# Performance work log

Measured on AMD Instinct MI355X. Metric: run time of the kernel, lower is better.

## Reference

```python
import jax, jax.numpy as jnp
import numpy as np

EPS = 1e-5
GROUPS = 32


def conv2d(x, w, b):
    # x: [N,C,H,W], w: [O,I,3,3] (or 1x1), stride 1, padding 'same' for 3x3
    kh = w.shape[2]
    pad = (kh - 1) // 2
    y = jax.lax.conv_general_dilated(x, w, (1, 1), ((pad, pad), (pad, pad)),
                                     dimension_numbers=('NCHW', 'OIHW', 'NCHW'))
    return y + b[None, :, None, None]


def group_norm(x, g, b):
    N, C, H, W = x.shape
    xr = x.reshape(N, GROUPS, C // GROUPS, H, W)
    mu = xr.mean(axis=(2, 3, 4), keepdims=True)
    var = xr.var(axis=(2, 3, 4), keepdims=True)
    xr = (xr - mu) / jnp.sqrt(var + EPS)
    return xr.reshape(N, C, H, W) * g[None, :, None, None] + b[None, :, None, None]


def batch_norm(x, g, b):
    # training-mode BatchNorm2d: batch statistics over (N,H,W)
    mu = x.mean(axis=(0, 2, 3), keepdims=True)
    var = x.var(axis=(0, 2, 3), keepdims=True)
    return (x - mu) / jnp.sqrt(var + EPS) * g[None, :, None, None] + b[None, :, None, None]


def binary_activation(x):
    # STE: forward sign(x), backward through piecewise poly out3
    out_fwd = jnp.sign(x)
    m1 = (x < -1).astype(x.dtype)
    m2 = (x < 0).astype(x.dtype)
    m3 = (x < 1).astype(x.dtype)
    out1 = -1.0 * m1 + (x * x + 2.0 * x) * (1.0 - m1)
    out2 = out1 * m2 + (-x * x + 2.0 * x) * (1.0 - m2)
    out3 = out2 * m3 + 1.0 * (1.0 - m3)
    return jax.lax.stop_gradient(out_fwd - out3) + out3


def hard_binary_conv(x, w, b):
    # per-output-channel scaling * sign(w), STE through clipped weights
    scale = jax.lax.stop_gradient(jnp.mean(jnp.abs(w), axis=(1, 2, 3), keepdims=True))
    bw_ng = scale * jnp.sign(w)
    clipped = jnp.clip(w, -1.0, 1.0)
    bw = jax.lax.stop_gradient(bw_ng - clipped) + clipped
    return conv2d(x, bw, b)


def learnable_bias(x, emb, w, b):
    bias = jax.nn.silu(emb) @ w.T + b  # [B, C]
    return x + bias[:, :, None, None]


def _forward(c, x, emb,
             rb_gn1_g, rb_gn1_b, rb_conv1_w, rb_conv1_b, rb_emb_w, rb_emb_b,
             rb_gn2_g, rb_gn2_b, rb_conv2_w, rb_conv2_b,
             m1_w, m1_b, bconv_w, bconv_b, bn_g, bn_b,
             m2_w, m2_b, prelu_a, m3_w, m3_b):
    # ResBlock (skip = Identity since out_channels == channels)
    h = conv2d(jax.nn.silu(group_norm(c, rb_gn1_g, rb_gn1_b)), rb_conv1_w, rb_conv1_b)
    eo = jax.nn.silu(emb) @ rb_emb_w.T + rb_emb_b          # [B, 2*C]
    scale, shift = jnp.split(eo[:, :, None, None], 2, axis=1)
    h = group_norm(h, rb_gn2_g, rb_gn2_b) * (1.0 + scale) + shift
    h = conv2d(jax.nn.silu(h), rb_conv2_w, rb_conv2_b)
    c2 = c + h
    # concat + bias + STE binarize + binary conv + BN + channel-pool residual + PReLU
    xc = jnp.concatenate([x, c2], axis=1)                   # [B, 2C, H, W]
    out = learnable_bias(xc, emb, m1_w, m1_b)
    out = binary_activation(out)
    out = hard_binary_conv(out, bconv_w, bconv_b)
    out = batch_norm(out, bn_g, bn_b)
    N, C2, H, W = xc.shape
    out = out + xc.reshape(N, C2 // 2, 2, H, W).mean(axis=2)  # channel mean pooling
    out = learnable_bias(out, emb, m2_w, m2_b)
    out = jnp.where(out >= 0, out, prelu_a[None, :, None, None] * out)  # PReLU
    out = learnable_bias(out, emb, m3_w, m3_b)
    return out


def setup_inputs() -> dict:
    key = jax.random.key(0)
    ks = jax.random.split(key, 24)
    B, C, EMB, H, W = 8, 128, 512, 64, 64
    IN2 = 2 * C
    n = lambda k, s, sc=0.05: jax.random.normal(k, s, dtype=jnp.float32) * sc
    return {
        'c': jax.random.normal(ks[0], (B, C, H, W), dtype=jnp.float32),
        'x': jax.random.normal(ks[1], (B, C, H, W), dtype=jnp.float32),
        'emb': jax.random.normal(ks[2], (B, EMB), dtype=jnp.float32),
        'rb_gn1_g': jnp.ones((C,), jnp.float32), 'rb_gn1_b': jnp.zeros((C,), jnp.float32),
        'rb_conv1_w': n(ks[3], (C, C, 3, 3)), 'rb_conv1_b': n(ks[4], (C,)),
        'rb_emb_w': n(ks[5], (2 * C, EMB)), 'rb_emb_b': n(ks[6], (2 * C,)),
        'rb_gn2_g': jnp.ones((C,), jnp.float32), 'rb_gn2_b': jnp.zeros((C,), jnp.float32),
        'rb_conv2_w': n(ks[7], (C, C, 3, 3)), 'rb_conv2_b': n(ks[8], (C,)),
        'm1_w': n(ks[9], (IN2, EMB)), 'm1_b': n(ks[10], (IN2,)),
        'bconv_w': jax.random.uniform(ks[11], (C, IN2, 3, 3), dtype=jnp.float32) * 0.001,
        'bconv_b': n(ks[12], (C,)),
        'bn_g': jnp.ones((C,), jnp.float32), 'bn_b': jnp.zeros((C,), jnp.float32),
        'm2_w': n(ks[13], (C, EMB)), 'm2_b': n(ks[14], (C,)),
        'prelu_a': jnp.full((C,), 0.25, jnp.float32),
        'm3_w': n(ks[15], (C, EMB)), 'm3_b': n(ks[16], (C,)),
    }


def reference(c, x, emb,
              rb_gn1_g, rb_gn1_b, rb_conv1_w, rb_conv1_b, rb_emb_w, rb_emb_b,
              rb_gn2_g, rb_gn2_b, rb_conv2_w, rb_conv2_b,
              m1_w, m1_b, bconv_w, bconv_b, bn_g, bn_b,
              m2_w, m2_b, prelu_a, m3_w, m3_b):
    return _forward(c, x, emb,
                    rb_gn1_g, rb_gn1_b, rb_conv1_w, rb_conv1_b, rb_emb_w, rb_emb_b,
                    rb_gn2_g, rb_gn2_b, rb_conv2_w, rb_conv2_b,
                    m1_w, m1_b, bconv_w, bconv_b, bn_g, bn_b,
                    m2_w, m2_b, prelu_a, m3_w, m3_b)
```

## Files before the change

kernel.cpp:

```cpp
#include <hip/hip_runtime.h>
#include <stdint.h>


#define B_   8
#define C_   128
#define C2_  256
#define HW_  4096
#define EMB_ 512
#define EPS_ 1e-5f

typedef int   v16i __attribute__((ext_vector_type(16)));
typedef float v16f __attribute__((ext_vector_type(16)));
typedef short v8s  __attribute__((ext_vector_type(8)));
typedef int   v4i  __attribute__((ext_vector_type(4)));

#define COLB 272
#define LDSZ (3 * 66 * COLB)

__device__ __forceinline__ float silu(float v) { return v / (1.f + expf(-v)); }
__device__ __forceinline__ unsigned short f2bf(float f) {
    unsigned int x = __float_as_uint(f);
    return (unsigned short)((x + 0x7FFFu + ((x >> 16) & 1u)) >> 16);
}
__device__ __forceinline__ int8_t sgn8(float v) {
    return (v > 0.f) ? (int8_t)1 : ((v < 0.f) ? (int8_t)(-1) : (int8_t)0);
}

__global__ __launch_bounds__(256) void k_prep(
    const float* __restrict__ w, int8_t* __restrict__ sgn,
    float* __restrict__ alpha, float* __restrict__ bnS, float* __restrict__ bnQ,
    float* __restrict__ gnS, float* __restrict__ gnQ,
    const float* __restrict__ w1, const float* __restrict__ w2,
    unsigned short* __restrict__ Wc1, unsigned short* __restrict__ Wc2,
    const float* __restrict__ emb,
    const float* __restrict__ ew, const float* __restrict__ ebb,
    const float* __restrict__ m1w, const float* __restrict__ m1b,
    const float* __restrict__ m2w, const float* __restrict__ m2b,
    const float* __restrict__ m3w, const float* __restrict__ m3b,
    float* __restrict__ eo, float* __restrict__ b1,
    float* __restrict__ b2, float* __restrict__ b3) {
    __shared__ float red[256];
    const int blk = blockIdx.x, tid = threadIdx.x;
    if (blk < 128) {
        const int o = blk;
        if (o == 0 && tid < 128) { bnS[tid] = 0.f; bnQ[tid] = 0.f; }
        if (o == 1) { gnS[tid] = 0.f; }
        if (o == 2) { gnQ[tid] = 0.f; }
        const float* wr = w + (size_t)o * (C2_ * 9);
        float s = 0.f;
        for (int i = tid; i < C2_ * 9; i += 256) s += fabsf(wr[i]);
        red[tid] = s;
        __syncthreads();
        for (int st = 128; st > 0; st >>= 1) {
            if (tid < st) red[tid] += red[tid + st];
            __syncthreads();
        }
        if (tid == 0) alpha[o] = red[0] / (float)(C2_ * 9);
        for (int kk = 0; kk < 9; ++kk) {
            float v = wr[tid * 9 + kk];
            sgn[((size_t)(kk * 16 + (tid >> 4)) * C_ + o) * 16 + (tid & 15)] = sgn8(v);
        }
    } else if (blk < 704) {
        int i = (blk - 128) * 256 + tid;
        int co = i / (C_ * 9);
        int rem = i - co * (C_ * 9);
        int ci = rem / 9, kk = rem - ci * 9;
        size_t d = ((size_t)(kk * 16 + (ci >> 3)) * C_ + co) * 8 + (ci & 7);
        Wc1[d] = f2bf(w1[i]);
        Wc2[d] = f2bf(w2[i]);
    } else {
        const int o = (blk - 704) * 4 + (tid >> 6);
        const int l = tid & 63;
        const float* wv;
        float bias;
        float* dst;
        int dstride;
        if (o < 256)      { wv = ew  + (size_t)o * EMB_;              bias = ebb[o];    dst = eo + o;  dstride = 256; }
        else if (o < 512) { int r = o - 256; wv = m1w + (size_t)r * EMB_; bias = m1b[r]; dst = b1 + r; dstride = 256; }
        else if (o < 640) { int r = o - 512; wv = m2w + (size_t)r * EMB_; bias = m2b[r]; dst = b2 + r; dstride = 128; }
        else              { int r = o - 640; wv = m3w + (size_t)r * EMB_; bias = m3b[r]; dst = b3 + r; dstride = 128; }
        const float4 wa = *(const float4*)(wv + 8 * l);
        const float4 wb = *(const float4*)(wv + 8 * l + 4);
#pragma unroll
        for (int b = 0; b < B_; ++b) {
            const float* s = emb + b * EMB_ + 8 * l;
            float4 sa = *(const float4*)(s);
            float4 sb = *(const float4*)(s + 4);
            float p = wa.x * silu(sa.x) + wa.y * silu(sa.y) + wa.z * silu(sa.z) + wa.w * silu(sa.w) +
                      wb.x * silu(sb.x) + wb.y * silu(sb.y) + wb.z * silu(sb.z) + wb.w * silu(sb.w);
#pragma unroll
            for (int off = 32; off > 0; off >>= 1) p += __shfl_down(p, off, 64);
            if (l == 0) dst[b * dstride] = bias + p;
        }
    }
}

__global__ __launch_bounds__(1024) void k_gn1t(const float* __restrict__ in,
                                               const float* __restrict__ g,
                                               const float* __restrict__ b,
                                               unsigned short* __restrict__ act) {
    __shared__ float ssum[1024], ssq[1024];
    __shared__ float s_mu, s_rstd;
    const int tid = threadIdx.x;
    const int n = blockIdx.x >> 5, grp = blockIdx.x & 31;
    const size_t base = ((size_t)(n * C_ + grp * 4)) << 12;
    float sum = 0.f, sq = 0.f;
    const float4* in4 = (const float4*)(in + base);
    for (int i = tid; i < 4096; i += 1024) {
        float4 v = in4[i];
        sum += v.x + v.y + v.z + v.w;
        sq += v.x * v.x + v.y * v.y + v.z * v.z + v.w * v.w;
    }
    ssum[tid] = sum; ssq[tid] = sq;
    __syncthreads();
    for (int st = 512; st > 0; st >>= 1) {
        if (tid < st) { ssum[tid] += ssum[tid + st]; ssq[tid] += ssq[tid + st]; }
        __syncthreads();
    }
    if (tid == 0) {
        float mu = ssum[0] * (1.f / 16384.f);
        float var = ssq[0] * (1.f / 16384.f) - mu * mu;
        s_mu = mu; s_rstd = rsqrtf(var + EPS_);
    }
    __syncthreads();
    const float mu = s_mu, rstd = s_rstd;
    float gg[4], bb[4];
#pragma unroll
    for (int j = 0; j < 4; ++j) { gg[j] = g[grp * 4 + j]; bb[j] = b[grp * 4 + j]; }
    for (int hw = tid; hw < HW_; hw += 1024) {
        union { unsigned short u[4]; uint2 v; } pk;
#pragma unroll
        for (int j = 0; j < 4; ++j) {
            float v = in[base + ((size_t)j << 12) + hw];
            pk.u[j] = f2bf(silu((v - mu) * rstd * gg[j] + bb[j]));
        }
        *(uint2*)(act + ((size_t)(n * HW_ + hw)) * C_ + grp * 4) = pk.v;
    }
}

__global__ __launch_bounds__(1024) void k_gn2a(const float* __restrict__ in,
                                               const float* __restrict__ g,
                                               const float* __restrict__ b,
                                               const float* __restrict__ eo,
                                               const float* __restrict__ gnS,
                                               const float* __restrict__ gnQ,
                                               unsigned short* __restrict__ act) {
    const int tid = threadIdx.x;
    const int n = blockIdx.x >> 5, grp = blockIdx.x & 31;
    const size_t base = ((size_t)(n * C_ + grp * 4)) << 12;
    const float mu = gnS[n * 32 + grp] * (1.f / 16384.f);
    const float var = gnQ[n * 32 + grp] * (1.f / 16384.f) - mu * mu;
    const float rstd = rsqrtf(var + EPS_);
    float sc[4], sh[4], gg[4], bb[4];
#pragma unroll
    for (int j = 0; j < 4; ++j) {
        int ch = grp * 4 + j;
        gg[j] = g[ch]; bb[j] = b[ch];
        sc[j] = 1.f + eo[n * 256 + ch];
        sh[j] = eo[n * 256 + 128 + ch];
    }
    for (int hw = tid; hw < HW_; hw += 1024) {
        union { unsigned short u[4]; uint2 v; } pk;
#pragma unroll
        for (int j = 0; j < 4; ++j) {
            float v = in[base + ((size_t)j << 12) + hw];
            float y = ((v - mu) * rstd * gg[j] + bb[j]) * sc[j] + sh[j];
            pk.u[j] = f2bf(silu(y));
        }
        *(uint2*)(act + ((size_t)(n * HW_ + hw)) * C_ + grp * 4) = pk.v;
    }
}

__device__ __forceinline__ void stage_rows(char* lds, const char* rs0,
                                           const char* rs1, const char* rs2) {
    const int tid = threadIdx.x;
    const char* rs[3] = {rs0, rs1, rs2};
    if (tid < 96) {
        int r = tid / 32, q = tid & 31;
        int c = (q >> 4) ? 65 : 0, o = q & 15;
        *(float4*)(lds + (r * 66 + c) * COLB + o * 16) = make_float4(0.f, 0.f, 0.f, 0.f);
    }
#pragma unroll
    for (int u = 0; u < 12; ++u) {
        int idx = u * 256 + tid;
        int r = idx >> 10, rem = idx & 1023;
        int x = rem >> 4, o = rem & 15;
        char* dst = lds + (r * 66 + x + 1) * COLB + o * 16;
        if (rs[r]) *(float4*)dst = *(const float4*)(rs[r] + x * 256 + o * 16);
        else       *(float4*)dst = make_float4(0.f, 0.f, 0.f, 0.f);
    }
}

__global__ __launch_bounds__(256) void k_conv1(const unsigned short* __restrict__ act,
                                               const unsigned short* __restrict__ Wc,
                                               const float* __restrict__ bias,
                                               float* __restrict__ out,
                                               float* __restrict__ gnS,
                                               float* __restrict__ gnQ) {
    __shared__ __align__(16) char lds[LDSZ];
    const int y = blockIdx.x;
    const int n = blockIdx.y;
    const char* base = (const char*)(act + ((size_t)n * 64) * 64 * C_);
    stage_rows(lds,
               (y > 0)  ? base + (size_t)(y - 1) * 16384 : nullptr,
               base + (size_t)y * 16384,
               (y < 63) ? base + (size_t)(y + 1) * 16384 : nullptr);
    __syncthreads();

    const int w = threadIdx.x >> 6;
    const int l = threadIdx.x & 63;
    const int lm = l & 31;
    const int lh = l >> 5;

    v16f acc0, acc1;
#pragma unroll
    for (int i = 0; i < 16; ++i) { acc0[i] = 0.f; acc1[i] = 0.f; }

#pragma unroll
    for (int kk = 0; kk < 9; ++kk) {
        const int r = kk / 3, dx = kk % 3 - 1;
        const char* col0 = lds + (r * 66 + lm + 1 + dx) * COLB + 16 * lh;
        const char* col1 = col0 + 32 * COLB;
        const unsigned short* wbase = Wc + (size_t)(kk * 16 + lh) * C_ * 8 + (32 * w + lm) * 8;
#pragma unroll
        for (int cb = 0; cb < 8; ++cb) {
            v8s a = *(const v8s*)(wbase + (size_t)(2 * cb) * C_ * 8);
            v8s b0 = *(const v8s*)(col0 + 32 * cb);
            v8s b1 = *(const v8s*)(col1 + 32 * cb);
            acc0 = __builtin_amdgcn_mfma_f32_32x32x16_bf16(a, b0, acc0, 0, 0, 0);
            acc1 = __builtin_amdgcn_mfma_f32_32x32x16_bf16(a, b1, acc1, 0, 0, 0);
        }
    }
    float pr[16], qr[16];
#pragma unroll
    for (int r = 0; r < 16; ++r) {
        const int row = (r & 3) + 8 * (r >> 2) + 4 * lh;
        const int co = 32 * w + row;
        const float bv = bias[co];
        const size_t o = (((size_t)n * C_ + co) << 12) + (y << 6);
        float v0 = acc0[r] + bv, v1 = acc1[r] + bv;
        out[o + lm] = v0;
        out[o + 32 + lm] = v1;
        pr[r] = v0 + v1;
        qr[r] = v0 * v0 + v1 * v1;
    }
    __syncthreads();
    float* ldsS = (float*)lds;
    float* ldsQ = (float*)lds + 128;
#pragma unroll
    for (int r = 0; r < 16; ++r) {
        float p = pr[r], q = qr[r];
#pragma unroll
        for (int m = 16; m > 0; m >>= 1) {
            p += __shfl_xor(p, m, 64);
            q += __shfl_xor(q, m, 64);
        }
        if (lm == 0) {
            const int row = (r & 3) + 8 * (r >> 2) + 4 * lh;
            const int co = 32 * w + row;
            ldsS[co] = p;
            ldsQ[co] = q;
        }
    }
    __syncthreads();
    if (threadIdx.x < 32) {
        const int g = threadIdx.x;
        float p = ldsS[4 * g] + ldsS[4 * g + 1] + ldsS[4 * g + 2] + ldsS[4 * g + 3];
        float q = ldsQ[4 * g] + ldsQ[4 * g + 1] + ldsQ[4 * g + 2] + ldsQ[4 * g + 3];
        atomicAdd(&gnS[n * 32 + g], p);
        atomicAdd(&gnQ[n * 32 + g], q);
    }
}

__global__ __launch_bounds__(256) void k_conv2(const unsigned short* __restrict__ act,
                                               const unsigned short* __restrict__ Wc,
                                               const float* __restrict__ bias,
                                               const float* __restrict__ res,
                                               const float* __restrict__ xin,
                                               const float* __restrict__ b1v,
                                               float* __restrict__ out,
                                               int8_t* __restrict__ S) {
    __shared__ __align__(16) char lds[LDSZ];
    const int y = blockIdx.x;
    const int n = blockIdx.y;
    const char* base = (const char*)(act + ((size_t)n * 64) * 64 * C_);
    stage_rows(lds,
               (y > 0)  ? base + (size_t)(y - 1) * 16384 : nullptr,
               base + (size_t)y * 16384,
               (y < 63) ? base + (size_t)(y + 1) * 16384 : nullptr);
    __syncthreads();

    const int w = threadIdx.x >> 6;
    const int l = threadIdx.x & 63;
    const int lm = l & 31;
    const int lh = l >> 5;

    v16f acc0, acc1;
#pragma unroll
    for (int i = 0; i < 16; ++i) { acc0[i] = 0.f; acc1[i] = 0.f; }

#pragma unroll
    for (int kk = 0; kk < 9; ++kk) {
        const int r = kk / 3, dx = kk % 3 - 1;
        const char* col0 = lds + (r * 66 + lm + 1 + dx) * COLB + 16 * lh;
        const char* col1 = col0 + 32 * COLB;
        const unsigned short* wbase = Wc + (size_t)(kk * 16 + lh) * C_ * 8 + (32 * w + lm) * 8;
#pragma unroll
        for (int cb = 0; cb < 8; ++cb) {
            v8s a = *(const v8s*)(wbase + (size_t)(2 * cb) * C_ * 8);
            v8s b0 = *(const v8s*)(col0 + 32 * cb);
            v8s b1 = *(const v8s*)(col1 + 32 * cb);
            acc0 = __builtin_amdgcn_mfma_f32_32x32x16_bf16(a, b0, acc0, 0, 0, 0);
            acc1 = __builtin_amdgcn_mfma_f32_32x32x16_bf16(a, b1, acc1, 0, 0, 0);
        }
    }
    float c2v0[16], c2v1[16];
#pragma unroll
    for (int r = 0; r < 16; ++r) {
        const int row = (r & 3) + 8 * (r >> 2) + 4 * lh;
        const int co = 32 * w + row;
        const float bv = bias[co];
        const size_t o = (((size_t)n * C_ + co) << 12) + (y << 6);
        float v0 = acc0[r] + bv + res[o + lm];
        float v1 = acc1[r] + bv + res[o + 32 + lm];
        out[o + lm] = v0;
        out[o + 32 + lm] = v1;
        c2v0[r] = v0;
        c2v1[r] = v1;
    }

    __syncthreads();
#pragma unroll
    for (int q = 0; q < 4; ++q) {
        const int co0 = 32 * w + 8 * q + 4 * lh;
        const float b0 = b1v[n * 256 + 128 + co0];
        const float b1b = b1v[n * 256 + 128 + co0 + 1];
        const float b2b = b1v[n * 256 + 128 + co0 + 2];
        const float b3b = b1v[n * 256 + 128 + co0 + 3];
        union { int8_t b[4]; int u; } p0, p1;
        p0.b[0] = sgn8(c2v0[4 * q] + b0);  p1.b[0] = sgn8(c2v1[4 * q] + b0);
        p0.b[1] = sgn8(c2v0[4 * q + 1] + b1b); p1.b[1] = sgn8(c2v1[4 * q + 1] + b1b);
        p0.b[2] = sgn8(c2v0[4 * q + 2] + b2b); p1.b[2] = sgn8(c2v1[4 * q + 2] + b2b);
        p0.b[3] = sgn8(c2v0[4 * q + 3] + b3b); p1.b[3] = sgn8(c2v1[4 * q + 3] + b3b);
        *(int*)(lds + lm * COLB + 128 + co0) = p0.u;
        *(int*)(lds + (32 + lm) * COLB + 128 + co0) = p1.u;
    }
#pragma unroll
    for (int u = 0; u < 8; ++u) {
        int idx = u * 256 + threadIdx.x;
        int ch = idx >> 4, seg = idx & 15;
        float4 v = *(const float4*)(xin + (((size_t)(n * C_ + ch)) << 12) + (y << 6) + 4 * seg);
        const float bv = b1v[n * 256 + ch];
        lds[(4 * seg) * COLB + ch]     = sgn8(v.x + bv);
        lds[(4 * seg + 1) * COLB + ch] = sgn8(v.y + bv);
        lds[(4 * seg + 2) * COLB + ch] = sgn8(v.z + bv);
        lds[(4 * seg + 3) * COLB + ch] = sgn8(v.w + bv);
    }
    __syncthreads();
    int8_t* Srow = S + ((size_t)(n * HW_) + (y << 6)) * C2_;
#pragma unroll
    for (int u = 0; u < 4; ++u) {
        int idx = u * 256 + threadIdx.x;
        int px = idx >> 4, c16 = idx & 15;
        *(int4*)(Srow + (size_t)px * C2_ + 16 * c16) = *(const int4*)(lds + px * COLB + 16 * c16);
    }
}

__global__ __launch_bounds__(256) void k_bconv(const int8_t* __restrict__ S,
                                               const int8_t* __restrict__ Wk,
                                               const float* __restrict__ alpha,
                                               const float* __restrict__ bias,
                                               float* __restrict__ out,
                                               float* __restrict__ bnS,
                                               float* __restrict__ bnQ) {
    __shared__ __align__(16) char lds[LDSZ];
    const int y = blockIdx.x;
    const int n = blockIdx.y;
    const char* base = (const char*)(S + ((size_t)n * 64) * 64 * C2_);
    stage_rows(lds,
               (y > 0)  ? base + (size_t)(y - 1) * 16384 : nullptr,
               base + (size_t)y * 16384,
               (y < 63) ? base + (size_t)(y + 1) * 16384 : nullptr);
    __syncthreads();

    const int w = threadIdx.x >> 6;
    const int l = threadIdx.x & 63;
    const int lm = l & 31;
    const int lh = l >> 5;

    v16i acc0, acc1;
#pragma unroll
    for (int i = 0; i < 16; ++i) { acc0[i] = 0; acc1[i] = 0; }

#pragma unroll
    for (int kk = 0; kk < 9; ++kk) {
        const int r = kk / 3, dx = kk % 3 - 1;
        const char* col0 = lds + (r * 66 + lm + 1 + dx) * COLB + 16 * lh;
        const char* col1 = col0 + 32 * COLB;
        const int8_t* wbase = Wk + (size_t)(kk * 16 + lh) * C_ * 16 + (32 * w + lm) * 16;
#pragma unroll
        for (int s = 0; s < 8; ++s) {
            v4i a = *(const v4i*)(wbase + (size_t)(2 * s) * C_ * 16);
            v4i b0 = *(const v4i*)(col0 + 32 * s);
            v4i b1 = *(const v4i*)(col1 + 32 * s);
            acc0 = __builtin_amdgcn_mfma_i32_32x32x32_i8(a, b0, acc0, 0, 0, 0);
            acc1 = __builtin_amdgcn_mfma_i32_32x32x32_i8(a, b1, acc1, 0, 0, 0);
        }
    }

    float pr[16], qr[16];
#pragma unroll
    for (int r = 0; r < 16; ++r) {
        const int row = (r & 3) + 8 * (r >> 2) + 4 * lh;
        const int co = 32 * w + row;
        const float av = alpha[co], bv = bias[co];
        const size_t o = (((size_t)n * C_ + co) << 12) + (y << 6);
        float v0 = av * (float)acc0[r] + bv;
        float v1 = av * (float)acc1[r] + bv;
        out[o + lm]      = v0;
        out[o + 32 + lm] = v1;
        pr[r] = v0 + v1;
        qr[r] = v0 * v0 + v1 * v1;
    }
    __syncthreads();
    float* ldsS = (float*)lds;
    float* ldsQ = (float*)lds + 128;
#pragma unroll
    for (int r = 0; r < 16; ++r) {
        float p = pr[r], q = qr[r];
#pragma unroll
        for (int m = 16; m > 0; m >>= 1) {
            p += __shfl_xor(p, m, 64);
            q += __shfl_xor(q, m, 64);
        }
        if (lm == 0) {
            const int row = (r & 3) + 8 * (r >> 2) + 4 * lh;
            const int co = 32 * w + row;
            ldsS[co] = p;
            ldsQ[co] = q;
        }
    }
    __syncthreads();
    if (threadIdx.x < 128) {
        atomicAdd(&bnS[threadIdx.x], ldsS[threadIdx.x]);
        atomicAdd(&bnQ[threadIdx.x], ldsQ[threadIdx.x]);
    }
}

__global__ __launch_bounds__(256) void k_final(const float* __restrict__ y3,
                                               const float* __restrict__ x,
                                               const float* __restrict__ c2,
                                               const float* __restrict__ bnS,
                                               const float* __restrict__ bnQ,
                                               const float* __restrict__ bng,
                                               const float* __restrict__ bnb,
                                               const float* __restrict__ b2v,
                                               const float* __restrict__ pa,
                                               const float* __restrict__ b3v,
                                               float* __restrict__ out) {
    const int idx4 = blockIdx.x * 256 + threadIdx.x;
    const int hw = (idx4 & 1023) * 4;
    const int cb = idx4 >> 10;
    const int co = cb & 127;
    const int n = cb >> 7;
    const float mu = bnS[co] * (1.f / 32768.f);
    const float var = bnQ[co] * (1.f / 32768.f) - mu * mu;
    const float rstd = rsqrtf(var + EPS_);
    const float gm = rstd * bng[co];
    const float bt = bnb[co] - mu * gm;
    const size_t obase = (((size_t)(n * C_ + co)) << 12) + hw;
    float4 v = *(const float4*)(y3 + obase);
    v.x = v.x * gm + bt; v.y = v.y * gm + bt; v.z = v.z * gm + bt; v.w = v.w * gm + bt;

    const int ch0 = 2 * co;
    float4 pA, pB;
    if (co < 64) {
        pA = *(const float4*)(x + (((size_t)(n * C_ + ch0)) << 12) + hw);
        pB = *(const float4*)(x + (((size_t)(n * C_ + ch0 + 1)) << 12) + hw);
    } else {
        int d = ch0 - 128;
        pA = *(const float4*)(c2 + (((size_t)(n * C_ + d)) << 12) + hw);
        pB = *(const float4*)(c2 + (((size_t)(n * C_ + d + 1)) << 12) + hw);
    }
    const float bias2 = b2v[n * 128 + co];
    const float aP = pa[co];
    const float bias3 = b3v[n * 128 + co];
    float4 r;
    float t;
    t = v.x + 0.5f * (pA.x + pB.x) + bias2; t = (t >= 0.f) ? t : aP * t; r.x = t + bias3;
    t = v.y + 0.5f * (pA.y + pB.y) + bias2; t = (t >= 0.f) ? t : aP * t; r.y = t + bias3;
    t = v.z + 0.5f * (pA.z + pB.z) + bias2; t = (t >= 0.f) ? t : aP * t; r.z = t + bias3;
    t = v.w + 0.5f * (pA.w + pB.w) + bias2; t = (t >= 0.f) ? t : aP * t; r.w = t + bias3;
    *(float4*)(out + obase) = r;
}

extern "C" void kernel_launch(void* const* d_in, const int* in_sizes, int n_in,
                              void* d_out, int out_size, void* d_ws, size_t ws_size,
                              hipStream_t stream) {
    const float* c       = (const float*)d_in[0];
    const float* x       = (const float*)d_in[1];
    const float* emb     = (const float*)d_in[2];
    const float* gn1_g   = (const float*)d_in[3];
    const float* gn1_b   = (const float*)d_in[4];
    const float* conv1_w = (const float*)d_in[5];
    const float* conv1_b = (const float*)d_in[6];
    const float* emb_w   = (const float*)d_in[7];
    const float* emb_b   = (const float*)d_in[8];
    const float* gn2_g   = (const float*)d_in[9];
    const float* gn2_b   = (const float*)d_in[10];
    const float* conv2_w = (const float*)d_in[11];
    const float* conv2_b = (const float*)d_in[12];
    const float* m1_w    = (const float*)d_in[13];
    const float* m1_b    = (const float*)d_in[14];
    const float* bconv_w = (const float*)d_in[15];
    const float* bconv_b = (const float*)d_in[16];
    const float* bn_g    = (const float*)d_in[17];
    const float* bn_b    = (const float*)d_in[18];
    const float* m2_w    = (const float*)d_in[19];
    const float* m2_b    = (const float*)d_in[20];
    const float* prelu_a = (const float*)d_in[21];
    const float* m3_w    = (const float*)d_in[22];
    const float* m3_b    = (const float*)d_in[23];
    float* out = (float*)d_out;

    float* ws = (float*)d_ws;
    const size_t NCHW = (size_t)B_ * C_ * HW_;
    float*  a_buf = ws;
    float*  y_buf = ws + NCHW;
    unsigned short* actA = (unsigned short*)(ws + 2 * NCHW);
    int8_t* S     = (int8_t*)(ws + 2 * NCHW);
    int8_t* sgn   = (int8_t*)(ws + 2 * NCHW + NCHW / 2);
    unsigned short* Wc1 = (unsigned short*)(ws + 2 * NCHW + NCHW / 2 + 73728);
    unsigned short* Wc2 = Wc1 + C_ * C_ * 9;
    float*  alpha = ws + 2 * NCHW + NCHW / 2 + 73728 + 2 * 73728;
    float*  eo    = alpha + 128;
    float*  b1v   = eo + B_ * 256;
    float*  b2v   = b1v + B_ * 256;
    float*  b3v   = b2v + B_ * 128;
    float*  bnS   = b3v + B_ * 128;
    float*  bnQ   = bnS + 128;
    float*  gnS   = bnQ + 128;
    float*  gnQ   = gnS + 256;

    k_prep<<<896, 256, 0, stream>>>(bconv_w, sgn, alpha, bnS, bnQ, gnS, gnQ,
                                    conv1_w, conv2_w, Wc1, Wc2,
                                    emb, emb_w, emb_b, m1_w, m1_b, m2_w, m2_b,
                                    m3_w, m3_b, eo, b1v, b2v, b3v);
    k_gn1t<<<B_ * 32, 1024, 0, stream>>>(c, gn1_g, gn1_b, actA);
    k_conv1<<<dim3(64, B_), 256, 0, stream>>>(actA, Wc1, conv1_b, y_buf, gnS, gnQ);
    k_gn2a<<<B_ * 32, 1024, 0, stream>>>(y_buf, gn2_g, gn2_b, eo, gnS, gnQ, actA);
    k_conv2<<<dim3(64, B_), 256, 0, stream>>>(actA, Wc2, conv2_b, c, x, b1v, a_buf, S);
    k_bconv<<<dim3(64, B_), 256, 0, stream>>>(S, sgn, alpha, bconv_b, y_buf, bnS, bnQ);
    k_final<<<NCHW / 1024, 256, 0, stream>>>(y_buf, x, a_buf, bnS, bnQ, bn_g, bn_b,
                                             b2v, prelu_a, b3v, out);
}
```

Before: 257.7 us.

## Fuse GroupNorm kernels into prep and conv2 staging, store pooled conv2 output

GroupNorm1+SiLU moves into extra blocks of the prep kernel. GroupNorm2 with its emb modulation and SiLU is folded into conv2's LDS staging, which reads fp32 conv1 output directly, so two launches and an intermediate bf16 activation round-trip go away. Conv2 now writes a channel-pair-pooled half-size buffer instead of the full output, and SiLU uses a fast exp and reciprocal. Risks: the gn1 blocks in prep now run alongside the weight repacking, conv2 staging does more strided fp32 loads, and the fast-math SiLU is slightly less accurate.

```diff
diff --git a/kernel.cpp b/kernel.cpp
--- a/kernel.cpp
+++ b/kernel.cpp
@@ -17,7 +17,9 @@
 #define COLB 272
 #define LDSZ (3 * 66 * COLB)
 
-__device__ __forceinline__ float silu(float v) { return v / (1.f + expf(-v)); }
+__device__ __forceinline__ float silu(float v) {
+    return v * __builtin_amdgcn_rcpf(1.f + __expf(-v));
+}
 __device__ __forceinline__ unsigned short f2bf(float f) {
     unsigned int x = __float_as_uint(f);
     return (unsigned short)((x + 0x7FFFu + ((x >> 16) & 1u)) >> 16);
@@ -38,7 +40,9 @@
     const float* __restrict__ m2w, const float* __restrict__ m2b,
     const float* __restrict__ m3w, const float* __restrict__ m3b,
     float* __restrict__ eo, float* __restrict__ b1,
-    float* __restrict__ b2, float* __restrict__ b3) {
+    float* __restrict__ b2, float* __restrict__ b3,
+    const float* __restrict__ gin, const float* __restrict__ g1w,
+    const float* __restrict__ g1b, unsigned short* __restrict__ act1) {
     __shared__ float red[256];
     const int blk = blockIdx.x, tid = threadIdx.x;
     if (blk < 128) {
@@ -68,7 +72,7 @@
         size_t d = ((size_t)(kk * 16 + (ci >> 3)) * C_ + co) * 8 + (ci & 7);
         Wc1[d] = f2bf(w1[i]);
         Wc2[d] = f2bf(w2[i]);
-    } else {
+    } else if (blk < 896) {
         const int o = (blk - 704) * 4 + (tid >> 6);
         const int l = tid & 63;
         const float* wv;
@@ -92,82 +96,40 @@
             for (int off = 32; off > 0; off >>= 1) p += __shfl_down(p, off, 64);
             if (l == 0) dst[b * dstride] = bias + p;
         }
-    }
-}
-
-__global__ __launch_bounds__(1024) void k_gn1t(const float* __restrict__ in,
-                                               const float* __restrict__ g,
-                                               const float* __restrict__ b,
-                                               unsigned short* __restrict__ act) {
-    __shared__ float ssum[1024], ssq[1024];
-    __shared__ float s_mu, s_rstd;
-    const int tid = threadIdx.x;
-    const int n = blockIdx.x >> 5, grp = blockIdx.x & 31;
-    const size_t base = ((size_t)(n * C_ + grp * 4)) << 12;
-    float sum = 0.f, sq = 0.f;
-    const float4* in4 = (const float4*)(in + base);
-    for (int i = tid; i < 4096; i += 1024) {
-        float4 v = in4[i];
-        sum += v.x + v.y + v.z + v.w;
-        sq += v.x * v.x + v.y * v.y + v.z * v.z + v.w * v.w;
-    }
-    ssum[tid] = sum; ssq[tid] = sq;
-    __syncthreads();
-    for (int st = 512; st > 0; st >>= 1) {
-        if (tid < st) { ssum[tid] += ssum[tid + st]; ssq[tid] += ssq[tid + st]; }
+    } else {
+        const int bb = blk - 896;
+        const int n = bb >> 5, grp = bb & 31;
+        const size_t base = ((size_t)(n * C_ + grp * 4)) << 12;
+        float sum = 0.f, sq = 0.f;
+        const float4* in4 = (const float4*)(gin + base);
+        for (int i = tid; i < 4096; i += 256) {
+            float4 v = in4[i];
+            sum += v.x + v.y + v.z + v.w;
+            sq += v.x * v.x + v.y * v.y + v.z * v.z + v.w * v.w;
+        }
+#pragma unroll
+        for (int off = 32; off > 0; off >>= 1) {
+            sum += __shfl_xor(sum, off, 64);
+            sq  += __shfl_xor(sq, off, 64);
+        }
+        if ((tid & 63) == 0) { red[tid >> 6] = sum; red[8 + (tid >> 6)] = sq; }
         __syncthreads();
-    }
-    if (tid == 0) {
-        float mu = ssum[0] * (1.f / 16384.f);
-        float var = ssq[0] * (1.f / 16384.f) - mu * mu;
-        s_mu = mu; s_rstd = rsqrtf(var + EPS_);
-    }
-    __syncthreads();
-    const float mu = s_mu, rstd = s_rstd;
-    float gg[4], bb[4];
-#pragma unroll
-    for (int j = 0; j < 4; ++j) { gg[j] = g[grp * 4 + j]; bb[j] = b[grp * 4 + j]; }
-    for (int hw = tid; hw < HW_; hw += 1024) {
-        union { unsigned short u[4]; uint2 v; } pk;
-#pragma unroll
-        for (int j = 0; j < 4; ++j) {
-            float v = in[base + ((size_t)j << 12) + hw];
-            pk.u[j] = f2bf(silu((v - mu) * rstd * gg[j] + bb[j]));
-        }
-        *(uint2*)(act + ((size_t)(n * HW_ + hw)) * C_ + grp * 4) = pk.v;
-    }
-}
-
-__global__ __launch_bounds__(1024) void k_gn2a(const float* __restrict__ in,
-                                               const float* __restrict__ g,
-                                               const float* __restrict__ b,
-                                               const float* __restrict__ eo,
-                                               const float* __restrict__ gnS,
-                                               const float* __restrict__ gnQ,
-                                               unsigned short* __restrict__ act) {
-    const int tid = threadIdx.x;
-    const int n = blockIdx.x >> 5, grp = blockIdx.x & 31;
-    const size_t base = ((size_t)(n * C_ + grp * 4)) << 12;
-    const float mu = gnS[n * 32 + grp] * (1.f / 16384.f);
-    const float var = gnQ[n * 32 + grp] * (1.f / 16384.f) - mu * mu;
-    const float rstd = rsqrtf(var + EPS_);
-    float sc[4], sh[4], gg[4], bb[4];
-#pragma unroll
-    for (int j = 0; j < 4; ++j) {
-        int ch = grp * 4 + j;
-        gg[j] = g[ch]; bb[j] = b[ch];
-        sc[j] = 1.f + eo[n * 256 + ch];
-        sh[j] = eo[n * 256 + 128 + ch];
-    }
-    for (int hw = tid; hw < HW_; hw += 1024) {
-        union { unsigned short u[4]; uint2 v; } pk;
-#pragma unroll
-        for (int j = 0; j < 4; ++j) {
-            float v = in[base + ((size_t)j << 12) + hw];
-            float y = ((v - mu) * rstd * gg[j] + bb[j]) * sc[j] + sh[j];
-            pk.u[j] = f2bf(silu(y));
-        }
-        *(uint2*)(act + ((size_t)(n * HW_ + hw)) * C_ + grp * 4) = pk.v;
+        sum = red[0] + red[1] + red[2] + red[3];
+        sq  = red[8] + red[9] + red[10] + red[11];
+        const float mu = sum * (1.f / 16384.f);
+        const float rstd = rsqrtf(sq * (1.f / 16384.f) - mu * mu + EPS_);
+        float gg[4], bb4[4];
+#pragma unroll
+        for (int j = 0; j < 4; ++j) { gg[j] = g1w[grp * 4 + j]; bb4[j] = g1b[grp * 4 + j]; }
+        for (int hw = tid; hw < HW_; hw += 256) {
+            union { unsigned short u[4]; uint2 v; } pk;
+#pragma unroll
+            for (int j = 0; j < 4; ++j) {
+                float v = gin[base + ((size_t)j << 12) + hw];
+                pk.u[j] = f2bf(silu((v - mu) * rstd * gg[j] + bb4[j]));
+            }
+            *(uint2*)(act1 + ((size_t)(n * HW_ + hw)) * C_ + grp * 4) = pk.v;
+        }
     }
 }
 
@@ -272,26 +234,66 @@
     }
 }
 
-__global__ __launch_bounds__(256) void k_conv2(const unsigned short* __restrict__ act,
+__global__ __launch_bounds__(256) void k_conv2(const float* __restrict__ yin,
                                                const unsigned short* __restrict__ Wc,
                                                const float* __restrict__ bias,
                                                const float* __restrict__ res,
                                                const float* __restrict__ xin,
                                                const float* __restrict__ b1v,
-                                               float* __restrict__ out,
+                                               const float* __restrict__ eo,
+                                               const float* __restrict__ g2,
+                                               const float* __restrict__ bt2,
+                                               const float* __restrict__ gnS,
+                                               const float* __restrict__ gnQ,
+                                               float* __restrict__ poolC2,
                                                int8_t* __restrict__ S) {
     __shared__ __align__(16) char lds[LDSZ];
+    __shared__ float ldsA[128], ldsB[128];
     const int y = blockIdx.x;
     const int n = blockIdx.y;
-    const char* base = (const char*)(act + ((size_t)n * 64) * 64 * C_);
-    stage_rows(lds,
-               (y > 0)  ? base + (size_t)(y - 1) * 16384 : nullptr,
-               base + (size_t)y * 16384,
-               (y < 63) ? base + (size_t)(y + 1) * 16384 : nullptr);
-    __syncthreads();
-
-    const int w = threadIdx.x >> 6;
-    const int l = threadIdx.x & 63;
+    const int tid = threadIdx.x;
+
+    if (tid < 128) {
+        const int ch = tid, grp = tid >> 2;
+        const float mu = gnS[n * 32 + grp] * (1.f / 16384.f);
+        const float var = gnQ[n * 32 + grp] * (1.f / 16384.f) - mu * mu;
+        const float rstd = rsqrtf(var + EPS_);
+        const float gg = g2[ch] * rstd;
+        const float sc = 1.f + eo[n * 256 + ch];
+        ldsA[ch] = gg * sc;
+        ldsB[ch] = (bt2[ch] - mu * gg) * sc + eo[n * 256 + 128 + ch];
+    }
+    if (tid < 96) {
+        int r = tid / 32, q = tid & 31;
+        int cpad = (q >> 4) ? 65 : 0, o = q & 15;
+        *(float4*)(lds + (r * 66 + cpad) * COLB + o * 16) = make_float4(0.f, 0.f, 0.f, 0.f);
+    }
+    __syncthreads();
+
+    const float* yb = yin + ((size_t)n * C_) * HW_ + (y << 6);
+#pragma unroll 4
+    for (int u = 0; u < 24; ++u) {
+        int unit = u * 256 + tid;
+        int r = unit >> 11, rem = unit & 2047;
+        int ch = rem >> 4, seg = rem & 15;
+        int yy = y - 1 + r;
+        char* dst = lds + (r * 66 + 1 + seg) * COLB + ch * 2;
+        if (yy >= 0 && yy < 64) {
+            const float A = ldsA[ch], Bv = ldsB[ch];
+            const float* src = yb + (size_t)ch * HW_ + (r - 1) * 64 + seg;
+#pragma unroll
+            for (int j = 0; j < 4; ++j)
+                *(unsigned short*)(dst + (16 * j) * COLB) = f2bf(silu(src[16 * j] * A + Bv));
+        } else {
+#pragma unroll
+            for (int j = 0; j < 4; ++j)
+                *(unsigned short*)(dst + (16 * j) * COLB) = 0;
+        }
+    }
+    __syncthreads();
+
+    const int w = tid >> 6;
+    const int l = tid & 63;
     const int lm = l & 31;
     const int lh = l >> 5;
 
@@ -321,12 +323,17 @@
         const int co = 32 * w + row;
         const float bv = bias[co];
         const size_t o = (((size_t)n * C_ + co) << 12) + (y << 6);
-        float v0 = acc0[r] + bv + res[o + lm];
-        float v1 = acc1[r] + bv + res[o + 32 + lm];
-        out[o + lm] = v0;
-        out[o + 32 + lm] = v1;
-        c2v0[r] = v0;
-        c2v1[r] = v1;
+        c2v0[r] = acc0[r] + bv + res[o + lm];
+        c2v1[r] = acc1[r] + bv + res[o + 32 + lm];
+    }
+#pragma unroll
+    for (int q = 0; q < 4; ++q) {
+        const int pc = 16 * w + 4 * q + 2 * lh;
+        const size_t po = (((size_t)n * 64 + pc) << 12) + (y << 6);
+        poolC2[po + lm]             = 0.5f * (c2v0[4 * q] + c2v0[4 * q + 1]);
+        poolC2[po + 32 + lm]        = 0.5f * (c2v1[4 * q] + c2v1[4 * q + 1]);
+        poolC2[po + 4096 + lm]      = 0.5f * (c2v0[4 * q + 2] + c2v0[4 * q + 3]);
+        poolC2[po + 4096 + 32 + lm] = 0.5f * (c2v1[4 * q + 2] + c2v1[4 * q + 3]);
     }
 
     __syncthreads();
@@ -347,7 +354,7 @@
     }
 #pragma unroll
     for (int u = 0; u < 8; ++u) {
-        int idx = u * 256 + threadIdx.x;
+        int idx = u * 256 + tid;
         int ch = idx >> 4, seg = idx & 15;
         float4 v = *(const float4*)(xin + (((size_t)(n * C_ + ch)) << 12) + (y << 6) + 4 * seg);
         const float bv = b1v[n * 256 + ch];
@@ -360,7 +367,7 @@
     int8_t* Srow = S + ((size_t)(n * HW_) + (y << 6)) * C2_;
 #pragma unroll
     for (int u = 0; u < 4; ++u) {
-        int idx = u * 256 + threadIdx.x;
+        int idx = u * 256 + tid;
         int px = idx >> 4, c16 = idx & 15;
         *(int4*)(Srow + (size_t)px * C2_ + 16 * c16) = *(const int4*)(lds + px * COLB + 16 * c16);
     }
@@ -449,7 +456,7 @@
 
 __global__ __launch_bounds__(256) void k_final(const float* __restrict__ y3,
                                                const float* __restrict__ x,
-                                               const float* __restrict__ c2,
+                                               const float* __restrict__ poolC2,
                                                const float* __restrict__ bnS,
                                                const float* __restrict__ bnQ,
                                                const float* __restrict__ bng,
@@ -472,25 +479,25 @@
     float4 v = *(const float4*)(y3 + obase);
     v.x = v.x * gm + bt; v.y = v.y * gm + bt; v.z = v.z * gm + bt; v.w = v.w * gm + bt;
 
-    const int ch0 = 2 * co;
-    float4 pA, pB;
+    float4 pv;
     if (co < 64) {
-        pA = *(const float4*)(x + (((size_t)(n * C_ + ch0)) << 12) + hw);
-        pB = *(const float4*)(x + (((size_t)(n * C_ + ch0 + 1)) << 12) + hw);
+        const int ch0 = 2 * co;
+        float4 pA = *(const float4*)(x + (((size_t)(n * C_ + ch0)) << 12) + hw);
+        float4 pB = *(const float4*)(x + (((size_t)(n * C_ + ch0 + 1)) << 12) + hw);
+        pv.x = 0.5f * (pA.x + pB.x); pv.y = 0.5f * (pA.y + pB.y);
+        pv.z = 0.5f * (pA.z + pB.z); pv.w = 0.5f * (pA.w + pB.w);
     } else {
-        int d = ch0 - 128;
-        pA = *(const float4*)(c2 + (((size_t)(n * C_ + d)) << 12) + hw);
-        pB = *(const float4*)(c2 + (((size_t)(n * C_ + d + 1)) << 12) + hw);
+        pv = *(const float4*)(poolC2 + (((size_t)(n * 64 + co - 64)) << 12) + hw);
     }
     const float bias2 = b2v[n * 128 + co];
     const float aP = pa[co];
     const float bias3 = b3v[n * 128 + co];
     float4 r;
     float t;
-    t = v.x + 0.5f * (pA.x + pB.x) + bias2; t = (t >= 0.f) ? t : aP * t; r.x = t + bias3;
-    t = v.y + 0.5f * (pA.y + pB.y) + bias2; t = (t >= 0.f) ? t : aP * t; r.y = t + bias3;
-    t = v.z + 0.5f * (pA.z + pB.z) + bias2; t = (t >= 0.f) ? t : aP * t; r.z = t + bias3;
-    t = v.w + 0.5f * (pA.w + pB.w) + bias2; t = (t >= 0.f) ? t : aP * t; r.w = t + bias3;
+    t = v.x + pv.x + bias2; t = (t >= 0.f) ? t : aP * t; r.x = t + bias3;
+    t = v.y + pv.y + bias2; t = (t >= 0.f) ? t : aP * t; r.y = t + bias3;
+    t = v.z + pv.z + bias2; t = (t >= 0.f) ? t : aP * t; r.z = t + bias3;
+    t = v.w + pv.w + bias2; t = (t >= 0.f) ? t : aP * t; r.w = t + bias3;
     *(float4*)(out + obase) = r;
 }
 
@@ -525,7 +532,7 @@
 
     float* ws = (float*)d_ws;
     const size_t NCHW = (size_t)B_ * C_ * HW_;
-    float*  a_buf = ws;
+    float*  poolC2 = ws;
     float*  y_buf = ws + NCHW;
     unsigned short* actA = (unsigned short*)(ws + 2 * NCHW);
     int8_t* S     = (int8_t*)(ws + 2 * NCHW);
@@ -542,15 +549,15 @@
     float*  gnS   = bnQ + 128;
     float*  gnQ   = gnS + 256;
 
-    k_prep<<<896, 256, 0, stream>>>(bconv_w, sgn, alpha, bnS, bnQ, gnS, gnQ,
-                                    conv1_w, conv2_w, Wc1, Wc2,
-                                    emb, emb_w, emb_b, m1_w, m1_b, m2_w, m2_b,
-                                    m3_w, m3_b, eo, b1v, b2v, b3v);
-    k_gn1t<<<B_ * 32, 1024, 0, stream>>>(c, gn1_g, gn1_b, actA);
+    k_prep<<<1152, 256, 0, stream>>>(bconv_w, sgn, alpha, bnS, bnQ, gnS, gnQ,
+                                     conv1_w, conv2_w, Wc1, Wc2,
+                                     emb, emb_w, emb_b, m1_w, m1_b, m2_w, m2_b,
+                                     m3_w, m3_b, eo, b1v, b2v, b3v,
+                                     c, gn1_g, gn1_b, actA);
     k_conv1<<<dim3(64, B_), 256, 0, stream>>>(actA, Wc1, conv1_b, y_buf, gnS, gnQ);
-    k_gn2a<<<B_ * 32, 1024, 0, stream>>>(y_buf, gn2_g, gn2_b, eo, gnS, gnQ, actA);
-    k_conv2<<<dim3(64, B_), 256, 0, stream>>>(actA, Wc2, conv2_b, c, x, b1v, a_buf, S);
+    k_conv2<<<dim3(64, B_), 256, 0, stream>>>(y_buf, Wc2, conv2_b, c, x, b1v, eo,
+                                              gn2_g, gn2_b, gnS, gnQ, poolC2, S);
     k_bconv<<<dim3(64, B_), 256, 0, stream>>>(S, sgn, alpha, bconv_b, y_buf, bnS, bnQ);
-    k_final<<<NCHW / 1024, 256, 0, stream>>>(y_buf, x, a_buf, bnS, bnQ, bn_g, bn_b,
+    k_final<<<NCHW / 1024, 256, 0, stream>>>(y_buf, x, poolC2, bnS, bnQ, bn_g, bn_b,
                                              b2v, prelu_a, b3v, out);
 }
```

Measured after the change: 237.4 us. -7.9%, faster.
